# Optimization experiments

Measured on AMD Instinct MI355X. Metric: run time of the kernel, lower is better.

Reference implementation:

```python
import jax, jax.numpy as jnp
import numpy as np

B, T, P, D, H = 16, 512, 576, 1024, 16
HD = D // H  # head_dim = 64
SCALE = 1.0 / np.sqrt(HD).astype(np.float32)


def _split_heads(x):
    # [B, S, D] -> [B, H, S, HD]
    b, s, _ = x.shape
    return x.reshape(b, s, H, HD).transpose(0, 2, 1, 3)


def _merge_heads(x):
    # [B, H, S, HD] -> [B, S, D]
    b, h, s, hd = x.shape
    return x.transpose(0, 2, 1, 3).reshape(b, s, h * hd)


def _linear(x, w, b):
    # torch nn.Linear: y = x @ W^T + b, W is [out, in]
    return jnp.einsum('bsd,od->bso', x, w) + b


def setup_inputs() -> dict:
    key = jax.random.key(0)
    ks = jax.random.split(key, 12)
    inp = {
        'text_feats': jax.random.normal(ks[0], (B, T, D), jnp.float32),
        'image_feats': jax.random.normal(ks[1], (B, P, D), jnp.float32),
        'text_mask': jnp.ones((B, T), dtype=bool),
    }
    names = ['qt', 'ki', 'vi', 'qi', 'kt', 'vt', 'ot', 'oi']
    for i, n in enumerate(names):
        inp['w_' + n] = jax.random.normal(ks[2 + i], (D, D), jnp.float32) * 0.02
        inp['b_' + n] = jnp.zeros((D,), jnp.float32)
    return inp


def reference(text_feats, image_feats, text_mask,
              w_qt, b_qt, w_ki, b_ki, w_vi, b_vi,
              w_qi, b_qi, w_kt, b_kt, w_vt, b_vt,
              w_ot, b_ot, w_oi, b_oi):
    # ---- text attends to image (no mask on image keys) ----
    q_t = _split_heads(_linear(text_feats, w_qt, b_qt))    # [B,H,T,HD]
    k_i = _split_heads(_linear(image_feats, w_ki, b_ki))   # [B,H,P,HD]
    v_i = _split_heads(_linear(image_feats, w_vi, b_vi))   # [B,H,P,HD]
    scores_ti = jnp.einsum('bhtd,bhpd->bhtp', q_t, k_i) * SCALE
    attn_ti = jax.nn.softmax(scores_ti, axis=-1)
    text_attended = _merge_heads(jnp.einsum('bhtp,bhpd->bhtd', attn_ti, v_i))
    text_attended = _linear(text_attended, w_ot, b_ot)

    # ---- image attends to text (mask on text keys) ----
    q_i = _split_heads(_linear(image_feats, w_qi, b_qi))   # [B,H,P,HD]
    k_t = _split_heads(_linear(text_feats, w_kt, b_kt))    # [B,H,T,HD]
    v_t = _split_heads(_linear(text_feats, w_vt, b_vt))    # [B,H,T,HD]
    scores_it = jnp.einsum('bhpd,bhtd->bhpt', q_i, k_t) * SCALE
    scores_it = jnp.where(text_mask[:, None, None, :], scores_it, -jnp.inf)
    attn_it = jax.nn.softmax(scores_it, axis=-1)
    image_attended = _merge_heads(jnp.einsum('bhpt,bhtd->bhpd', attn_it, v_t))
    image_attended = _linear(image_attended, w_oi, b_oi)

    return (text_attended, image_attended)
```

## Files before the change

### kernel.cpp

```cpp
#include <hip/hip_runtime.h>
#include <stdint.h>

typedef unsigned short u16;
typedef __bf16 bf16x8 __attribute__((ext_vector_type(8)));
typedef float f32x4 __attribute__((ext_vector_type(4)));

#define SCALE_QK 0.125f

__device__ __forceinline__ u16 f2bf(float f) {
    uint32_t u = __builtin_bit_cast(uint32_t, f);
    u += 0x7FFFu + ((u >> 16) & 1u);
    return (u16)(u >> 16);
}

__device__ __forceinline__ int bdiv(int x, int S) {
    return (S == 512) ? (x >> 9) : (int)(((uint64_t)(x >> 6) * 954437177ull) >> 33);
}

__device__ __forceinline__ void gload_lds16(const void* g, void* l) {
    __builtin_amdgcn_global_load_lds(
        (__attribute__((address_space(1))) void*)(g),
        (__attribute__((address_space(3))) void*)(l), 16, 0, 0);
}

__global__ void cvt_f32_bf16(const float* __restrict__ src, u16* __restrict__ dst, int n4) {
    int i = blockIdx.x * blockDim.x + threadIdx.x;
    if (i >= n4) return;
    float4 v = ((const float4*)src)[i];
    ushort4 o;
    o.x = f2bf(v.x); o.y = f2bf(v.y); o.z = f2bf(v.z); o.w = f2bf(v.w);
    ((ushort4*)dst)[i] = o;
}

struct Ptr8 { const float* p[8]; };

__global__ void cvt_w8(Ptr8 srcs, u16* __restrict__ dst) {
    int i = blockIdx.x * blockDim.x + threadIdx.x;
    int mat = i >> 18, off = i & 262143;
    float4 v = ((const float4*)srcs.p[mat])[off];
    ushort4 o;
    o.x = f2bf(v.x); o.y = f2bf(v.y); o.z = f2bf(v.z); o.w = f2bf(v.w);
    ((ushort4*)(dst + ((size_t)mat << 20)))[off] = o;
}

__global__ void prep(const int* __restrict__ maski, float* __restrict__ mb,
                     const float* __restrict__ bqt, const float* __restrict__ bkt,
                     const float* __restrict__ bqi, const float* __restrict__ bki,
                     float* __restrict__ biasbuf) {
    int i = blockIdx.x * blockDim.x + threadIdx.x;
    if (i < 8192) {
        int v0 = maski[0];
        int v = (v0 == 0x01010101) ? (int)((const unsigned char*)maski)[i] : maski[i];
        mb[i] = v ? 0.0f : -1e30f;
    } else if (i < 12288) {
        int j = i - 8192;
        float v = (j < 1024) ? bqt[j] : (j < 2048) ? bkt[j - 1024]
                : (j < 3072) ? bqi[j - 2048] : bki[j - 3072];
        biasbuf[j] = v;
    }
}

template<int LAYOUT>
__global__ __launch_bounds__(512)
void gemm256(const u16* __restrict__ A0, const u16* __restrict__ B0,
             const float* __restrict__ bias0, void* __restrict__ C0,
             int nx0, int S0, size_t pstr0, int nblk0,
             const u16* __restrict__ A1, const u16* __restrict__ B1,
             const float* __restrict__ bias1, void* __restrict__ C1,
             int nx1, int S1, size_t pstr1) {
    constexpr int K = 1024;
    constexpr int NT = K / 64;
    __shared__ u16 As[2][256 * 64];
    __shared__ u16 Bs[2][256 * 64];
    const int tid = threadIdx.x;
    const int wid = tid >> 6, lane = tid & 63;
    const int lo = lane & 15, hi = lane >> 4;
    const int wm = wid >> 2, wn = wid & 3;
    const int tot = (int)gridDim.x;
    int f = ((int)blockIdx.x & 7) * (tot >> 3) + ((int)blockIdx.x >> 3);
    const u16 *Ag, *Bg; const float* bias; void* Cg; int nx, S; size_t pstr;
    if (f < nblk0) { Ag = A0; Bg = B0; bias = bias0; Cg = C0; nx = nx0; S = S0; pstr = pstr0; }
    else { f -= nblk0; Ag = A1; Bg = B1; bias = bias1; Cg = C1; nx = nx1; S = S1; pstr = pstr1; }
    const int bm = f / nx, bn = f - bm * nx;
    const u16* Ab = Ag + (size_t)bm * 256 * K;
    const u16* Bb = Bg + (size_t)bn * 256 * K;

    const int srow = tid >> 3;
    const int sslot = (tid & 7) ^ (srow & 7);
    const int ldst = (tid >> 6) * 512;

    auto stageA = [&](int buf, int k0, int c) {
        gload_lds16(Ab + (size_t)(c * 64 + srow) * K + k0 + sslot * 8,
                    &As[buf][0] + c * 4096 + ldst);
    };
    auto stageB = [&](int buf, int k0, int c) {
        gload_lds16(Bb + (size_t)(c * 64 + srow) * K + k0 + sslot * 8,
                    &Bs[buf][0] + c * 4096 + ldst);
    };

    f32x4 acc[8][4] = {};

#pragma unroll
    for (int c = 0; c < 4; ++c) { stageA(0, 0, c); stageB(0, 0, c); }
    asm volatile("s_waitcnt vmcnt(0)" ::: "memory");
    __builtin_amdgcn_s_barrier();

    for (int t = 0; t < NT; ++t) {
        const int cur = t & 1;
        const int k0n = (t + 1) * 64;
        const u16* Atile = &As[cur][0];
        const u16* Btile = &Bs[cur][0];
#pragma unroll
        for (int ph = 0; ph < 4; ++ph) {
            const int ks = ph >> 1, mh = ph & 1;
            bf16x8 af[4], bq[4];
#pragma unroll
            for (int m = 0; m < 4; ++m) {
                int row = wm * 128 + mh * 64 + m * 16 + lo;
                af[m] = *(const bf16x8*)(Atile + row * 64 + (((ks * 4 + hi) ^ (row & 7)) << 3));
            }
#pragma unroll
            for (int n = 0; n < 4; ++n) {
                int row = wn * 64 + n * 16 + lo;
                bq[n] = *(const bf16x8*)(Btile + row * 64 + (((ks * 4 + hi) ^ (row & 7)) << 3));
            }
            if (t + 1 < NT) {
                if (ph == 0) {
#pragma unroll
                    for (int c = 0; c < 4; ++c) stageA(cur ^ 1, k0n, c);
                } else if (ph == 1) {
#pragma unroll
                    for (int c = 0; c < 4; ++c) stageB(cur ^ 1, k0n, c);
                }
            }
            __builtin_amdgcn_s_barrier();
            __builtin_amdgcn_s_setprio(1);
#pragma unroll
            for (int m = 0; m < 4; ++m)
#pragma unroll
                for (int n = 0; n < 4; ++n)
                    acc[mh * 4 + m][n] =
                        __builtin_amdgcn_mfma_f32_16x16x32_bf16(af[m], bq[n], acc[mh * 4 + m][n], 0, 0, 0);
            __builtin_amdgcn_s_setprio(0);
            if (ph < 3) {
                __builtin_amdgcn_s_barrier();
            } else {
                asm volatile("s_waitcnt vmcnt(0)" ::: "memory");
                __builtin_amdgcn_s_barrier();
            }
        }
    }

    const int rowbase = bm * 256 + wm * 128, colbase = bn * 256 + wn * 64;

    if (LAYOUT == 0) {
        float* C = (float*)Cg;
#pragma unroll
        for (int m = 0; m < 8; ++m)
#pragma unroll
            for (int r = 0; r < 4; ++r) {
                int row = rowbase + m * 16 + hi * 4 + r;
#pragma unroll
                for (int n = 0; n < 4; ++n) {
                    int col = colbase + n * 16 + lo;
                    C[(size_t)row * 1024 + col] = acc[m][n][r] + bias[col];
                }
            }
    } else if (LAYOUT == 1) {
#pragma unroll
        for (int m = 0; m < 8; ++m)
#pragma unroll
            for (int r = 0; r < 4; ++r) {
                int row = rowbase + m * 16 + hi * 4 + r;
                int b = bdiv(row, S);
                int s = row - b * S;
#pragma unroll
                for (int n = 0; n < 4; ++n) {
                    int cb = colbase + n * 16;
                    int part = cb >> 10, h = (cb >> 6) & 15;
                    u16* bp = (u16*)Cg + (size_t)part * pstr +
                              (((size_t)(b * 16 + h) * S + s) << 6) + (cb & 63) + lo;
                    *bp = f2bf(acc[m][n][r] + bias[cb + lo]);
                }
            }
    } else {
        u16* base = (u16*)Cg;
        int bn_[4], s0_[4];
#pragma unroll
        for (int n = 0; n < 4; ++n) {
            int col0 = colbase + n * 16;
            int b = bdiv(col0, S);
            bn_[n] = b;
            s0_[n] = col0 - b * S;
        }
#pragma unroll
        for (int m = 0; m < 8; ++m)
#pragma unroll
            for (int r = 0; r < 4; ++r) {
                int dout = rowbase + m * 16 + hi * 4 + r;
                float bv = bias[dout];
#pragma unroll
                for (int n = 0; n < 4; ++n)
                    base[((size_t)bn_[n] * 1024 + dout) * S + s0_[n] + lo] =
                        f2bf(acc[m][n][r] + bv);
            }
    }
}

template<int MASKED, int NQ, int SK>
__global__ __launch_bounds__(256)
void attn_v4(const u16* __restrict__ Q, const u16* __restrict__ Kb,
             const u16* __restrict__ Vt, const float* __restrict__ mb,
             u16* __restrict__ Out) {
    constexpr int SQ = NQ * 64;
    constexpr int NC = SK / 64;
    __shared__ u16 kls[2][64 * 64];
    __shared__ u16 vls[2][64 * 64];
    __shared__ u16 pls[4][16 * 72];
    const int tid = threadIdx.x, wid = tid >> 6, lane = tid & 63;
    const int lo = lane & 15, hi = lane >> 4;
    const int id = blockIdx.x;
    const int f = (id & 7) * (NQ * 32) + (id >> 3);
    const int qc = f % NQ, bh = f / NQ;
    const int b = bh >> 4, h = bh & 15;
    const int q0 = qc * 64 + wid * 16;
    const u16* Qp = Q + ((size_t)bh * SQ + q0) * 64;
    const u16* Kp = Kb + (size_t)bh * SK * 64;
    const u16* Vp = Vt + (size_t)bh * 64 * SK;

    bf16x8 qf[2];
#pragma unroll
    for (int ks = 0; ks < 2; ++ks)
        qf[ks] = *(const bf16x8*)(Qp + lo * 64 + ks * 32 + hi * 8);

    f32x4 oacc[4] = {};
    float m = -3e38f, l = 0.f;
    u16* pl = pls[wid];
    uint32_t* pl32 = (uint32_t*)pl;

    auto stage = [&](int bufi, int c0) {
#pragma unroll
        for (int j = 0; j < 2; ++j) {
            const int beta = (j * 4 + wid) * 64 + lane;
            const int row = beta >> 3, slot = beta & 7;
            const int e = (slot ^ (row & 7)) << 3;
            gload_lds16(Kp + (size_t)(c0 + row) * 64 + e,
                        &kls[bufi][0] + (j * 4 + wid) * 512);
            gload_lds16(Vp + (size_t)row * SK + c0 + e,
                        &vls[bufi][0] + (j * 4 + wid) * 512);
        }
    };

    stage(0, 0);
    __syncthreads();

    for (int c = 0; c < NC; ++c) {
        const int c0 = c * 64;
        if (c + 1 < NC) stage((c + 1) & 1, c0 + 64);
        const u16* kb = &kls[c & 1][0];
        const u16* vb = &vls[c & 1][0];

        float sc[4][4];
#pragma unroll
        for (int kt = 0; kt < 4; ++kt) {
            const int krow = kt * 16 + lo;
            const int rx = krow & 7;
            bf16x8 kf0 = *(const bf16x8*)(kb + krow * 64 + ((hi ^ rx) << 3));
            bf16x8 kf1 = *(const bf16x8*)(kb + krow * 64 + (((4 + hi) ^ rx) << 3));
            f32x4 z = {};
            __builtin_amdgcn_s_setprio(1);
            z = __builtin_amdgcn_mfma_f32_16x16x32_bf16(kf0, qf[0], z, 0, 0, 0);
            z = __builtin_amdgcn_mfma_f32_16x16x32_bf16(kf1, qf[1], z, 0, 0, 0);
            __builtin_amdgcn_s_setprio(0);
            if (MASKED) {
                float4 mv = *(const float4*)(mb + b * SK + c0 + kt * 16 + hi * 4);
#pragma unroll
                for (int r = 0; r < 4; ++r) sc[kt][r] = z[r] * SCALE_QK + ((const float*)&mv)[r];
            } else {
#pragma unroll
                for (int r = 0; r < 4; ++r) sc[kt][r] = z[r] * SCALE_QK;
            }
        }
        float a0 = fmaxf(fmaxf(sc[0][0], sc[0][1]), fmaxf(sc[0][2], sc[0][3]));
        float a1 = fmaxf(fmaxf(sc[1][0], sc[1][1]), fmaxf(sc[1][2], sc[1][3]));
        float a2 = fmaxf(fmaxf(sc[2][0], sc[2][1]), fmaxf(sc[2][2], sc[2][3]));
        float a3 = fmaxf(fmaxf(sc[3][0], sc[3][1]), fmaxf(sc[3][2], sc[3][3]));
        float pmax = fmaxf(fmaxf(a0, a1), fmaxf(a2, a3));
        pmax = fmaxf(pmax, __shfl_xor(pmax, 16));
        pmax = fmaxf(pmax, __shfl_xor(pmax, 32));
        if (!__all(pmax - m <= 8.0f)) {
            float mn = fmaxf(m, pmax);
            float alpha = __expf(m - mn);
            m = mn;
            l *= alpha;
#pragma unroll
            for (int n = 0; n < 4; ++n)
#pragma unroll
                for (int r = 0; r < 4; ++r) oacc[n][r] *= alpha;
        }
        float sum = 0.f;
#pragma unroll
        for (int kt = 0; kt < 4; ++kt) {
#pragma unroll
            for (int r = 0; r < 4; ++r) {
                float p = __expf(sc[kt][r] - m);
                sc[kt][r] = p;
                sum += p;
            }
        }
        sum += __shfl_xor(sum, 16);
        sum += __shfl_xor(sum, 32);
        l += sum;
#pragma unroll
        for (int kt = 0; kt < 4; ++kt) {
#pragma unroll
            for (int rp = 0; rp < 2; ++rp) {
                uint32_t w = (uint32_t)f2bf(sc[kt][2 * rp]) |
                             ((uint32_t)f2bf(sc[kt][2 * rp + 1]) << 16);
                pl32[lo * 36 + kt * 8 + hi * 2 + rp] = w;
            }
        }
        bf16x8 pf0 = *(const bf16x8*)(pl + lo * 72 + hi * 8);
        bf16x8 pf1 = *(const bf16x8*)(pl + lo * 72 + 32 + hi * 8);
        __builtin_amdgcn_s_setprio(1);
#pragma unroll
        for (int n = 0; n < 4; ++n) {
            const int d = n * 16 + lo;
            const int dx = d & 7;
            bf16x8 v0 = *(const bf16x8*)(vb + d * 64 + ((hi ^ dx) << 3));
            bf16x8 v1 = *(const bf16x8*)(vb + d * 64 + (((4 + hi) ^ dx) << 3));
            oacc[n] = __builtin_amdgcn_mfma_f32_16x16x32_bf16(v0, pf0, oacc[n], 0, 0, 0);
            oacc[n] = __builtin_amdgcn_mfma_f32_16x16x32_bf16(v1, pf1, oacc[n], 0, 0, 0);
        }
        __builtin_amdgcn_s_setprio(0);
        __syncthreads();
    }
    const float inv = 1.0f / l;
    u16* op = Out + ((size_t)(b * SQ + q0 + lo)) * 1024 + h * 64;
#pragma unroll
    for (int n = 0; n < 4; ++n) {
        ushort4 w;
        w.x = f2bf(oacc[n][0] * inv);
        w.y = f2bf(oacc[n][1] * inv);
        w.z = f2bf(oacc[n][2] * inv);
        w.w = f2bf(oacc[n][3] * inv);
        *(ushort4*)(op + n * 16 + hi * 4) = w;
    }
}

extern "C" void kernel_launch(void* const* d_in, const int* in_sizes, int n_in,
                              void* d_out, int out_size, void* d_ws, size_t ws_size,
                              hipStream_t stream) {
    (void)in_sizes; (void)n_in; (void)out_size; (void)ws_size;
    const float* text  = (const float*)d_in[0];
    const float* image = (const float*)d_in[1];
    const int*   maski = (const int*)d_in[2];
    const float* w_qt = (const float*)d_in[3];  const float* b_qt = (const float*)d_in[4];
    const float* w_ki = (const float*)d_in[5];  const float* b_ki = (const float*)d_in[6];
    const float* w_vi = (const float*)d_in[7];  const float* b_vi = (const float*)d_in[8];
    const float* w_qi = (const float*)d_in[9];  const float* b_qi = (const float*)d_in[10];
    const float* w_kt = (const float*)d_in[11]; const float* b_kt = (const float*)d_in[12];
    const float* w_vt = (const float*)d_in[13]; const float* b_vt = (const float*)d_in[14];
    const float* w_ot = (const float*)d_in[15]; const float* b_ot = (const float*)d_in[16];
    const float* w_oi = (const float*)d_in[17]; const float* b_oi = (const float*)d_in[18];

    const int B = 16, T = 512, P = 576, D = 1024;
    const int MT = B * T;
    const int MI = B * P;
    const size_t M1 = 1 << 20;

    char* wp = (char*)d_ws;
    auto alloc = [&](size_t bytes) { char* r = wp; wp += (bytes + 255) & ~(size_t)255; return r; };
    u16* Xt   = (u16*)alloc((size_t)MT * D * 2);
    u16* Xi   = (u16*)alloc((size_t)MI * D * 2);
    u16* Wall = (u16*)alloc(8 * M1 * 2);
    float* biasbuf = (float*)alloc(4096 * 4);
    float* mbf  = (float*)alloc((size_t)B * T * 4);
    u16* QKt  = (u16*)alloc((size_t)2 * MT * D * 2);
    u16* QKi  = (u16*)alloc((size_t)2 * MI * D * 2);
    u16* Vtt  = (u16*)alloc((size_t)MT * D * 2);
    u16* Vti  = (u16*)alloc((size_t)MI * D * 2);

    const u16* Wqk_t = Wall;
    const u16* Wqk_i = Wall + 2 * M1;
    const u16* Wv_t  = Wall + 4 * M1;
    const u16* Wv_i  = Wall + 5 * M1;
    const u16* Wot   = Wall + 6 * M1;
    const u16* Woi   = Wall + 7 * M1;

    cvt_f32_bf16<<<(MT * D / 4) / 256, 256, 0, stream>>>(text, Xt, MT * D / 4);
    cvt_f32_bf16<<<(MI * D / 4) / 256, 256, 0, stream>>>(image, Xi, MI * D / 4);
    Ptr8 w8 = {{w_qt, w_kt, w_qi, w_ki, w_vt, w_vi, w_ot, w_oi}};
    cvt_w8<<<8192, 256, 0, stream>>>(w8, Wall);
    prep<<<48, 256, 0, stream>>>(maski, mbf, b_qt, b_kt, b_qi, b_ki, biasbuf);

    gemm256<1><<<544, 512, 0, stream>>>(
        Xt, Wqk_t, biasbuf,        QKt, 8, T, (size_t)MT * D, 256,
        Xi, Wqk_i, biasbuf + 2048, QKi, 8, P, (size_t)MI * D);
    gemm256<2><<<272, 512, 0, stream>>>(
        Wv_t, Xt, b_vt, Vtt, 32, T, 0, 128,
        Wv_i, Xi, b_vi, Vti, 36, P, 0);

    attn_v4<0, 8, 576><<<8 * 256, 256, 0, stream>>>(
        QKt, QKi + (size_t)MI * D, Vti, nullptr, Xt);
    attn_v4<1, 9, 512><<<9 * 256, 256, 0, stream>>>(
        QKi, QKt + (size_t)MT * D, Vtt, mbf, Xi);

    gemm256<0><<<272, 512, 0, stream>>>(
        Xt, Wot, b_ot, d_out, 4, T, 0, 128,
        Xi, Woi, b_oi, (void*)((float*)d_out + (size_t)MT * D), 4, P, 0);
}
```

Measured before the change: 410.5 us.

## Deepen GEMM LDS pipeline to 4-stage ring and merge projection launches

The GEMM kernel now uses a 4-slot LDS ring of K=32 units holding A and B together, with three units in flight. Each unit waits with a partial vmcnt and takes one barrier, replacing the old double buffer that needed several barriers per K=64 tile. The Q/K and V projection GEMMs are merged into one 816-block launch driven by a segment table, so the output layout becomes a runtime branch. This aims to hide global load latency, cut barrier stalls and launch gaps. In exchange, all three epilogues compile into one kernel, which may raise register pressure.

Result: faster. 358.3 us (-12.7%).

```diff
diff --git a/kernel.cpp b/kernel.cpp
--- a/kernel.cpp
+++ b/kernel.cpp
@@ -17,10 +17,15 @@
     return (S == 512) ? (x >> 9) : (int)(((uint64_t)(x >> 6) * 954437177ull) >> 33);
 }
 
-__device__ __forceinline__ void gload_lds16(const void* g, void* l) {
+__device__ __forceinline__ void gload16(const void* g, void* l) {
     __builtin_amdgcn_global_load_lds(
         (__attribute__((address_space(1))) void*)(g),
         (__attribute__((address_space(3))) void*)(l), 16, 0, 0);
+}
+
+template<int W>
+__device__ __forceinline__ void vwait() {
+    asm volatile("s_waitcnt vmcnt(%0)" :: "n"(W) : "memory");
 }
 
 __global__ void cvt_f32_bf16(const float* __restrict__ src, u16* __restrict__ dst, int n4) {
@@ -60,101 +65,89 @@
     }
 }
 
-template<int LAYOUT>
-__global__ __launch_bounds__(512)
-void gemm256(const u16* __restrict__ A0, const u16* __restrict__ B0,
-             const float* __restrict__ bias0, void* __restrict__ C0,
-             int nx0, int S0, size_t pstr0, int nblk0,
-             const u16* __restrict__ A1, const u16* __restrict__ B1,
-             const float* __restrict__ bias1, void* __restrict__ C1,
-             int nx1, int S1, size_t pstr1) {
+struct Seg {
+    const u16* A; const u16* B; const float* bias; void* C;
+    int nx, S, layout, end; size_t pstr;
+};
+struct Segs { Seg s[4]; };
+
+__global__ __launch_bounds__(512, 2)
+void gemm256v2(Segs segs) {
     constexpr int K = 1024;
-    constexpr int NT = K / 64;
-    __shared__ u16 As[2][256 * 64];
-    __shared__ u16 Bs[2][256 * 64];
+    __shared__ u16 U[4][256 * 64];
     const int tid = threadIdx.x;
     const int wid = tid >> 6, lane = tid & 63;
     const int lo = lane & 15, hi = lane >> 4;
     const int wm = wid >> 2, wn = wid & 3;
     const int tot = (int)gridDim.x;
     int f = ((int)blockIdx.x & 7) * (tot >> 3) + ((int)blockIdx.x >> 3);
-    const u16 *Ag, *Bg; const float* bias; void* Cg; int nx, S; size_t pstr;
-    if (f < nblk0) { Ag = A0; Bg = B0; bias = bias0; Cg = C0; nx = nx0; S = S0; pstr = pstr0; }
-    else { f -= nblk0; Ag = A1; Bg = B1; bias = bias1; Cg = C1; nx = nx1; S = S1; pstr = pstr1; }
-    const int bm = f / nx, bn = f - bm * nx;
-    const u16* Ab = Ag + (size_t)bm * 256 * K;
-    const u16* Bb = Bg + (size_t)bn * 256 * K;
-
-    const int srow = tid >> 3;
-    const int sslot = (tid & 7) ^ (srow & 7);
-    const int ldst = (tid >> 6) * 512;
-
-    auto stageA = [&](int buf, int k0, int c) {
-        gload_lds16(Ab + (size_t)(c * 64 + srow) * K + k0 + sslot * 8,
-                    &As[buf][0] + c * 4096 + ldst);
+    int si = 0;
+    while (si < 3 && f >= segs.s[si].end) ++si;
+    if (si > 0) f -= segs.s[si - 1].end;
+    const Seg sg = segs.s[si];
+    const int bm = f / sg.nx, bn = f - bm * sg.nx;
+    const u16* Ab = sg.A + (size_t)bm * 256 * K;
+    const u16* Bb = sg.B + (size_t)bn * 256 * K;
+
+    const int srow8 = tid >> 3;
+    const int sslot = tid & 7;
+
+    auto stage_unit = [&](int u) {
+        const int reg = u & 3;
+        const int kb = u * 32;
+#pragma unroll
+        for (int c = 0; c < 4; ++c) {
+            int row = c * 64 + srow8;
+            int ss = sslot ^ (row & 7);
+            const u16* src = (ss < 4)
+                ? Ab + (size_t)row * K + kb + ss * 8
+                : Bb + (size_t)row * K + kb + (ss - 4) * 8;
+            gload16(src, &U[reg][0] + c * 4096 + wid * 512);
+        }
     };
-    auto stageB = [&](int buf, int k0, int c) {
-        gload_lds16(Bb + (size_t)(c * 64 + srow) * K + k0 + sslot * 8,
-                    &Bs[buf][0] + c * 4096 + ldst);
+
+    f32x4 acc[8][4] = {};
+
+    stage_unit(0); stage_unit(1); stage_unit(2);
+
+    auto phase = [&](int u, bool doStage) {
+        const u16* R = &U[u & 3][0];
+        bf16x8 af[8], bq[4];
+#pragma unroll
+        for (int m = 0; m < 8; ++m) {
+            int row = wm * 128 + m * 16 + lo;
+            af[m] = *(const bf16x8*)(R + row * 64 + ((hi ^ (row & 7)) << 3));
+        }
+#pragma unroll
+        for (int n = 0; n < 4; ++n) {
+            int row = wn * 64 + n * 16 + lo;
+            bq[n] = *(const bf16x8*)(R + row * 64 + (((4 + hi) ^ (row & 7)) << 3));
+        }
+        if (doStage) stage_unit(u + 3);
+        __builtin_amdgcn_s_setprio(1);
+#pragma unroll
+        for (int m = 0; m < 8; ++m)
+#pragma unroll
+            for (int n = 0; n < 4; ++n)
+                acc[m][n] = __builtin_amdgcn_mfma_f32_16x16x32_bf16(af[m], bq[n], acc[m][n], 0, 0, 0);
+        __builtin_amdgcn_s_setprio(0);
     };
 
-    f32x4 acc[8][4] = {};
-
-#pragma unroll
-    for (int c = 0; c < 4; ++c) { stageA(0, 0, c); stageB(0, 0, c); }
-    asm volatile("s_waitcnt vmcnt(0)" ::: "memory");
-    __builtin_amdgcn_s_barrier();
-
-    for (int t = 0; t < NT; ++t) {
-        const int cur = t & 1;
-        const int k0n = (t + 1) * 64;
-        const u16* Atile = &As[cur][0];
-        const u16* Btile = &Bs[cur][0];
-#pragma unroll
-        for (int ph = 0; ph < 4; ++ph) {
-            const int ks = ph >> 1, mh = ph & 1;
-            bf16x8 af[4], bq[4];
-#pragma unroll
-            for (int m = 0; m < 4; ++m) {
-                int row = wm * 128 + mh * 64 + m * 16 + lo;
-                af[m] = *(const bf16x8*)(Atile + row * 64 + (((ks * 4 + hi) ^ (row & 7)) << 3));
-            }
-#pragma unroll
-            for (int n = 0; n < 4; ++n) {
-                int row = wn * 64 + n * 16 + lo;
-                bq[n] = *(const bf16x8*)(Btile + row * 64 + (((ks * 4 + hi) ^ (row & 7)) << 3));
-            }
-            if (t + 1 < NT) {
-                if (ph == 0) {
-#pragma unroll
-                    for (int c = 0; c < 4; ++c) stageA(cur ^ 1, k0n, c);
-                } else if (ph == 1) {
-#pragma unroll
-                    for (int c = 0; c < 4; ++c) stageB(cur ^ 1, k0n, c);
-                }
-            }
-            __builtin_amdgcn_s_barrier();
-            __builtin_amdgcn_s_setprio(1);
-#pragma unroll
-            for (int m = 0; m < 4; ++m)
-#pragma unroll
-                for (int n = 0; n < 4; ++n)
-                    acc[mh * 4 + m][n] =
-                        __builtin_amdgcn_mfma_f32_16x16x32_bf16(af[m], bq[n], acc[mh * 4 + m][n], 0, 0, 0);
-            __builtin_amdgcn_s_setprio(0);
-            if (ph < 3) {
-                __builtin_amdgcn_s_barrier();
-            } else {
-                asm volatile("s_waitcnt vmcnt(0)" ::: "memory");
-                __builtin_amdgcn_s_barrier();
-            }
-        }
-    }
+#pragma unroll 4
+    for (int u = 0; u < 28; ++u) {
+        vwait<8>();
+        __builtin_amdgcn_s_barrier();
+        phase(u, true);
+    }
+    vwait<8>(); __builtin_amdgcn_s_barrier(); phase(28, true);
+    vwait<8>(); __builtin_amdgcn_s_barrier(); phase(29, false);
+    vwait<4>(); __builtin_amdgcn_s_barrier(); phase(30, false);
+    vwait<0>(); __builtin_amdgcn_s_barrier(); phase(31, false);
 
     const int rowbase = bm * 256 + wm * 128, colbase = bn * 256 + wn * 64;
 
-    if (LAYOUT == 0) {
-        float* C = (float*)Cg;
+    if (sg.layout == 0) {
+        float* C = (float*)sg.C;
 #pragma unroll
         for (int m = 0; m < 8; ++m)
 #pragma unroll
@@ -163,45 +156,45 @@
 #pragma unroll
                 for (int n = 0; n < 4; ++n) {
                     int col = colbase + n * 16 + lo;
-                    C[(size_t)row * 1024 + col] = acc[m][n][r] + bias[col];
+                    C[(size_t)row * 1024 + col] = acc[m][n][r] + sg.bias[col];
                 }
             }
-    } else if (LAYOUT == 1) {
+    } else if (sg.layout == 1) {
 #pragma unroll
         for (int m = 0; m < 8; ++m)
 #pragma unroll
             for (int r = 0; r < 4; ++r) {
                 int row = rowbase + m * 16 + hi * 4 + r;
-                int b = bdiv(row, S);
-                int s = row - b * S;
+                int b = bdiv(row, sg.S);
+                int s = row - b * sg.S;
 #pragma unroll
                 for (int n = 0; n < 4; ++n) {
                     int cb = colbase + n * 16;
                     int part = cb >> 10, h = (cb >> 6) & 15;
-                    u16* bp = (u16*)Cg + (size_t)part * pstr +
-                              (((size_t)(b * 16 + h) * S + s) << 6) + (cb & 63) + lo;
-                    *bp = f2bf(acc[m][n][r] + bias[cb + lo]);
+                    u16* bp = (u16*)sg.C + (size_t)part * sg.pstr +
+                              (((size_t)(b * 16 + h) * sg.S + s) << 6) + (cb & 63) + lo;
+                    *bp = f2bf(acc[m][n][r] + sg.bias[cb + lo]);
                 }
             }
     } else {
-        u16* base = (u16*)Cg;
+        u16* base = (u16*)sg.C;
         int bn_[4], s0_[4];
 #pragma unroll
         for (int n = 0; n < 4; ++n) {
             int col0 = colbase + n * 16;
-            int b = bdiv(col0, S);
+            int b = bdiv(col0, sg.S);
             bn_[n] = b;
-            s0_[n] = col0 - b * S;
+            s0_[n] = col0 - b * sg.S;
         }
 #pragma unroll
         for (int m = 0; m < 8; ++m)
 #pragma unroll
             for (int r = 0; r < 4; ++r) {
                 int dout = rowbase + m * 16 + hi * 4 + r;
-                float bv = bias[dout];
+                float bv = sg.bias[dout];
 #pragma unroll
                 for (int n = 0; n < 4; ++n)
-                    base[((size_t)bn_[n] * 1024 + dout) * S + s0_[n] + lo] =
+                    base[((size_t)bn_[n] * 1024 + dout) * sg.S + s0_[n] + lo] =
                         f2bf(acc[m][n][r] + bv);
             }
     }
@@ -244,10 +237,10 @@
             const int beta = (j * 4 + wid) * 64 + lane;
             const int row = beta >> 3, slot = beta & 7;
             const int e = (slot ^ (row & 7)) << 3;
-            gload_lds16(Kp + (size_t)(c0 + row) * 64 + e,
-                        &kls[bufi][0] + (j * 4 + wid) * 512);
-            gload_lds16(Vp + (size_t)row * SK + c0 + e,
-                        &vls[bufi][0] + (j * 4 + wid) * 512);
+            gload16(Kp + (size_t)(c0 + row) * 64 + e,
+                    &kls[bufi][0] + (j * 4 + wid) * 512);
+            gload16(Vp + (size_t)row * SK + c0 + e,
+                    &vls[bufi][0] + (j * 4 + wid) * 512);
         }
     };
 
@@ -394,19 +387,26 @@
     cvt_w8<<<8192, 256, 0, stream>>>(w8, Wall);
     prep<<<48, 256, 0, stream>>>(maski, mbf, b_qt, b_kt, b_qi, b_ki, biasbuf);
 
-    gemm256<1><<<544, 512, 0, stream>>>(
-        Xt, Wqk_t, biasbuf,        QKt, 8, T, (size_t)MT * D, 256,
-        Xi, Wqk_i, biasbuf + 2048, QKi, 8, P, (size_t)MI * D);
-    gemm256<2><<<272, 512, 0, stream>>>(
-        Wv_t, Xt, b_vt, Vtt, 32, T, 0, 128,
-        Wv_i, Xi, b_vi, Vti, 36, P, 0);
+    {
+        Segs sgs;
+        sgs.s[0] = {Xt,   Wqk_t, biasbuf,        QKt, 8,  512, 1, 256, (size_t)MT * D};
+        sgs.s[1] = {Xi,   Wqk_i, biasbuf + 2048, QKi, 8,  576, 1, 544, (size_t)MI * D};
+        sgs.s[2] = {Wv_t, Xt,    b_vt,           Vtt, 32, 512, 2, 672, 0};
+        sgs.s[3] = {Wv_i, Xi,    b_vi,           Vti, 36, 576, 2, 816, 0};
+        gemm256v2<<<816, 512, 0, stream>>>(sgs);
+    }
 
     attn_v4<0, 8, 576><<<8 * 256, 256, 0, stream>>>(
         QKt, QKi + (size_t)MI * D, Vti, nullptr, Xt);
     attn_v4<1, 9, 512><<<9 * 256, 256, 0, stream>>>(
         QKi, QKt + (size_t)MT * D, Vtt, mbf, Xi);
 
-    gemm256<0><<<272, 512, 0, stream>>>(
-        Xt, Wot, b_ot, d_out, 4, T, 0, 128,
-        Xi, Woi, b_oi, (void*)((float*)d_out + (size_t)MT * D), 4, P, 0);
-}
+    {
+        Segs sgs;
+        sgs.s[0] = {Xt, Wot, b_ot, d_out, 4, 512, 0, 128, 0};
+        sgs.s[1] = {Xi, Woi, b_oi, (void*)((float*)d_out + (size_t)MT * D), 4, 576, 0, 272, 0};
+        sgs.s[2] = sgs.s[1]; sgs.s[2].end = 272;
+        sgs.s[3] = sgs.s[1]; sgs.s[3].end = 272;
+        gemm256v2<<<272, 512, 0, stream>>>(sgs);
+    }
+}
```
